# Kernel tuning notes

Measured on AMD Instinct MI355X. Metric: run time of the kernel, lower is better.

The kernel has to match this reference:

```python
import jax, jax.numpy as jnp
import numpy as np

N_NODES = 100000
N_EDGES = 1600000
N_GRAPHS = 256
F_IN = 38
HID = 64


def graph_conv(x, edge_index, w_rel, b_rel, w_root):
    # PyG GraphConv (aggr='add'): out = lin_rel(sum_{j in N(i)} x_j) + lin_root(x_i)
    src, dst = edge_index[0], edge_index[1]
    agg = jax.ops.segment_sum(x[src], dst, num_segments=N_NODES)  # [N, F]
    return agg @ w_rel + b_rel + x @ w_root


def setup_inputs() -> dict:
    key = jax.random.key(0)
    ks = jax.random.split(key, 10)
    x = jax.random.normal(ks[0], (N_NODES, F_IN), dtype=jnp.float32)
    edge_index = jax.random.randint(ks[1], (2, N_EDGES), 0, N_NODES, dtype=jnp.int64)
    batch = jnp.sort(jax.random.randint(ks[2], (N_NODES,), 0, N_GRAPHS, dtype=jnp.int64))
    s1 = 1.0 / np.sqrt(F_IN)
    s2 = 1.0 / np.sqrt(HID)
    w1_rel = jax.random.uniform(ks[3], (F_IN, HID), jnp.float32, -s1, s1)
    b1_rel = jax.random.uniform(ks[4], (HID,), jnp.float32, -s1, s1)
    w1_root = jax.random.uniform(ks[5], (F_IN, HID), jnp.float32, -s1, s1)
    w2_rel = jax.random.uniform(ks[6], (HID, HID), jnp.float32, -s2, s2)
    b2_rel = jax.random.uniform(ks[7], (HID,), jnp.float32, -s2, s2)
    w2_root = jax.random.uniform(ks[8], (HID, HID), jnp.float32, -s2, s2)
    return {"x": x, "edge_index": edge_index, "batch": batch,
            "w1_rel": w1_rel, "b1_rel": b1_rel, "w1_root": w1_root,
            "w2_rel": w2_rel, "b2_rel": b2_rel, "w2_root": w2_root}


def reference(x, edge_index, batch, w1_rel, b1_rel, w1_root, w2_rel, b2_rel, w2_root):
    h = graph_conv(x, edge_index, w1_rel, b1_rel, w1_root)
    h = jax.nn.relu(h)
    h = graph_conv(h, edge_index, w2_rel, b2_rel, w2_root)
    # global_mean_pool: segment mean over batch ids
    sums = jax.ops.segment_sum(h, batch, num_segments=N_GRAPHS)  # [G, HID]
    counts = jax.ops.segment_sum(jnp.ones((N_NODES,), h.dtype), batch, num_segments=N_GRAPHS)
    pooled = sums / jnp.maximum(counts, 1.0)[:, None]
    # dropout(p=0.5, training=False) is identity in eval mode
    return jax.nn.relu(pooled)
```

## Files before the change

### kernel.cpp

```cpp
#include <hip/hip_runtime.h>

#define N_NODES 100000
#define N_EDGES 1600000
#define N_GRAPHS 256
#define F_IN 38
#define F_PAD 40
#define HID 64
#define CAPD 48

#define NB   391
#define EPB  4096
#define NBLK 391
#define BCAP 4608

typedef unsigned short ushort;
typedef unsigned int uint;
typedef _Float16 h2 __attribute__((ext_vector_type(2)));

__device__ __forceinline__ h2 u2h(uint u) {
    union { uint u; h2 h; } v; v.u = u; return v.h;
}
__device__ __forceinline__ uint h2u(h2 h) {
    union { uint u; h2 h; } v; v.h = h; return v.u;
}
__device__ __forceinline__ ushort f2h_bits(float f) {
    union { _Float16 h; ushort s; } v; v.h = (_Float16)f; return v.s;
}
__device__ __forceinline__ int clampi(int v) {
    return (int)min((uint)v, (uint)N_NODES);
}

__global__ void pack_x_kernel(const float* __restrict__ x,
                              ushort* __restrict__ xb,
                              ushort* __restrict__ hb) {
    int tid = blockIdx.x * blockDim.x + threadIdx.x;
    if (tid < HID) hb[(N_NODES << 6) + tid] = 0;
    if (tid >= (N_NODES + 1) * F_PAD) return;
    int n = tid / F_PAD;
    int f = tid - n * F_PAD;
    float v = (n < N_NODES && f < F_IN) ? x[n * F_IN + f] : 0.0f;
    xb[tid] = f2h_bits(v);
}

__global__ void scatter_kernel(const int* __restrict__ src,
                               const int* __restrict__ dst,
                               int* __restrict__ gcur,
                               uint2* __restrict__ ebuf) {
    __shared__ int hist[NB];
    __shared__ int cur[NB];
    for (int i = threadIdx.x; i < NB; i += 256) hist[i] = 0;
    __syncthreads();
    const int base = blockIdx.x * EPB;
    int d[EPB / 256];
    #pragma unroll
    for (int i = 0; i < EPB / 256; ++i) {
        int e = base + i * 256 + threadIdx.x;
        d[i] = (e < N_EDGES) ? dst[e] : -1;
        if (d[i] >= 0) atomicAdd(&hist[d[i] >> 8], 1);
    }
    __syncthreads();
    for (int i = threadIdx.x; i < NB; i += 256) {
        int c = hist[i];
        cur[i] = (c > 0) ? atomicAdd(&gcur[i], c) : 0;
    }
    __syncthreads();
    #pragma unroll
    for (int i = 0; i < EPB / 256; ++i) {
        int e = base + i * 256 + threadIdx.x;
        if (d[i] >= 0) {
            int b = d[i] >> 8;
            int pos = atomicAdd(&cur[b], 1);
            if (pos < BCAP) ebuf[b * BCAP + pos] = make_uint2((uint)src[e], (uint)d[i]);
        }
    }
}

__global__ void build_kernel(const uint2* __restrict__ ebuf,
                             const int* __restrict__ gcur,
                             int* __restrict__ cnt,
                             int* __restrict__ slots) {
    __shared__ int cl[256];
    const int b = blockIdx.x;
    cl[threadIdx.x] = 0;
    __syncthreads();
    int e1 = gcur[b]; if (e1 > BCAP) e1 = BCAP;
    for (int idx = threadIdx.x; idx < e1; idx += 256) {
        uint2 e = ebuf[b * BCAP + idx];
        int pos = atomicAdd(&cl[e.y & 255], 1);
        if (pos < CAPD) slots[(int)e.y * CAPD + pos] = (int)e.x;
    }
    __syncthreads();
    int n = (b << 8) + threadIdx.x;
    if (n < N_NODES) cnt[n] = cl[threadIdx.x];
}

__global__ __launch_bounds__(256, 4) void layer1_kernel(
        const uint* __restrict__ xb32,
        const int* __restrict__ cnt,
        const int* __restrict__ slots,
        const float* __restrict__ w_rel,
        const float* __restrict__ b_rel,
        const float* __restrict__ w_root,
        const int* __restrict__ batch,
        ushort* __restrict__ hb,
        float* __restrict__ hsum) {
    __shared__ uint s_wrelp[20 * HID];
    __shared__ uint s_wrootp[20 * HID];
    __shared__ uint s_a[64][20];
    __shared__ uint s_x[64][20];
    for (int i = threadIdx.x; i < 20 * HID; i += 256) {
        int kk = i >> 6, cc = i & 63;
        int k0 = 2 * kk, k1 = 2 * kk + 1;
        float r0 = (k0 < F_IN) ? w_rel[k0 * HID + cc] : 0.f;
        float r1 = (k1 < F_IN) ? w_rel[k1 * HID + cc] : 0.f;
        float o0 = (k0 < F_IN) ? w_root[k0 * HID + cc] : 0.f;
        float o1 = (k1 < F_IN) ? w_root[k1 * HID + cc] : 0.f;
        s_wrelp[i]  = (uint)f2h_bits(r0) | ((uint)f2h_bits(r1) << 16);
        s_wrootp[i] = (uint)f2h_bits(o0) | ((uint)f2h_bits(o1) << 16);
    }
    const int wave = threadIdx.x >> 6, lane = threadIdx.x & 63;
    const int base = blockIdx.x * 64;

    for (int i = 0; i < 16; ++i) {
        int nl = wave * 16 + i;
        int n = base + nl;
        uint xv = 0;
        int dp = 0;
        if (n < N_NODES) {
            int deg = cnt[n]; if (deg > CAPD) deg = CAPD;
            dp = (deg + 15) & ~15; if (dp > CAPD) dp = CAPD;
            if (lane < 20) xv = xb32[n * 20 + lane];
        }
        h2 sum = {(_Float16)0, (_Float16)0};
        const int* sl = slots + n * CAPD;
        for (int j = 0; j < dp; j += 16) {
            int4 a4 = *(const int4*)(sl + j);
            int4 b4 = *(const int4*)(sl + j + 4);
            int4 c4 = *(const int4*)(sl + j + 8);
            int4 d4 = *(const int4*)(sl + j + 12);
            if (lane < 20) {
                uint v0 = xb32[clampi(a4.x) * 20 + lane];
                uint v1 = xb32[clampi(a4.y) * 20 + lane];
                uint v2 = xb32[clampi(a4.z) * 20 + lane];
                uint v3 = xb32[clampi(a4.w) * 20 + lane];
                uint v4 = xb32[clampi(b4.x) * 20 + lane];
                uint v5 = xb32[clampi(b4.y) * 20 + lane];
                uint v6 = xb32[clampi(b4.z) * 20 + lane];
                uint v7 = xb32[clampi(b4.w) * 20 + lane];
                uint v8 = xb32[clampi(c4.x) * 20 + lane];
                uint v9 = xb32[clampi(c4.y) * 20 + lane];
                uint va = xb32[clampi(c4.z) * 20 + lane];
                uint vb = xb32[clampi(c4.w) * 20 + lane];
                uint vc = xb32[clampi(d4.x) * 20 + lane];
                uint vd = xb32[clampi(d4.y) * 20 + lane];
                uint ve = xb32[clampi(d4.z) * 20 + lane];
                uint vf = xb32[clampi(d4.w) * 20 + lane];
                h2 t0 = (u2h(v0) + u2h(v1)) + (u2h(v2) + u2h(v3));
                h2 t1 = (u2h(v4) + u2h(v5)) + (u2h(v6) + u2h(v7));
                h2 t2 = (u2h(v8) + u2h(v9)) + (u2h(va) + u2h(vb));
                h2 t3 = (u2h(vc) + u2h(vd)) + (u2h(ve) + u2h(vf));
                sum += (t0 + t1) + (t2 + t3);
            }
        }
        if (lane < 20) {
            s_a[nl][lane] = h2u(sum);
            s_x[nl][lane] = xv;
        }
    }
    __syncthreads();

    const int c = lane, r = wave;
    const float bias = b_rel[c];
    float psum = 0.f;
    int cur_g = -1;
    for (int i = 0; i < 16; ++i) {
        int nl = r * 16 + i;
        int n = base + nl;
        if (n >= N_NODES) break;
        h2 acc = {(_Float16)0, (_Float16)0};
        #pragma unroll
        for (int k8 = 0; k8 < 5; ++k8) {
            uint4 pa = *(const uint4*)&s_a[nl][k8 * 4];
            uint4 px = *(const uint4*)&s_x[nl][k8 * 4];
            acc += u2h(pa.x) * u2h(s_wrelp[(k8 * 4 + 0) * HID + c]);
            acc += u2h(pa.y) * u2h(s_wrelp[(k8 * 4 + 1) * HID + c]);
            acc += u2h(pa.z) * u2h(s_wrelp[(k8 * 4 + 2) * HID + c]);
            acc += u2h(pa.w) * u2h(s_wrelp[(k8 * 4 + 3) * HID + c]);
            acc += u2h(px.x) * u2h(s_wrootp[(k8 * 4 + 0) * HID + c]);
            acc += u2h(px.y) * u2h(s_wrootp[(k8 * 4 + 1) * HID + c]);
            acc += u2h(px.z) * u2h(s_wrootp[(k8 * 4 + 2) * HID + c]);
            acc += u2h(px.w) * u2h(s_wrootp[(k8 * 4 + 3) * HID + c]);
        }
        float hv = fmaxf((float)acc.x + (float)acc.y + bias, 0.f);
        hb[(n << 6) + c] = f2h_bits(hv);
        int g = batch[n];
        if (g != cur_g) {
            if (cur_g >= 0) atomicAdd(&hsum[(cur_g << 6) + c], psum);
            psum = 0.f;
            cur_g = g;
        }
        psum += hv;
    }
    if (cur_g >= 0) atomicAdd(&hsum[(cur_g << 6) + c], psum);
}

__global__ __launch_bounds__(256, 4) void layer2_kernel(
        const uint* __restrict__ hb32,
        const int* __restrict__ cnt,
        const int* __restrict__ slots,
        const int* __restrict__ batch,
        float* __restrict__ esum) {
    const int wave = threadIdx.x >> 6, lane = threadIdx.x & 63;
    const int base = blockIdx.x * 64;

    float psum0 = 0.f, psum1 = 0.f;
    int cur_g = -1;
    for (int i = 0; i < 16; ++i) {
        int n = base + wave * 16 + i;
        if (n >= N_NODES) break;
        int deg = cnt[n]; if (deg > CAPD) deg = CAPD;
        int dp = (deg + 15) & ~15; if (dp > CAPD) dp = CAPD;
        h2 sum = {(_Float16)0, (_Float16)0};
        const int* sl = slots + n * CAPD;
        for (int j = 0; j < dp; j += 16) {
            int4 a4 = *(const int4*)(sl + j);
            int4 b4 = *(const int4*)(sl + j + 4);
            int4 c4 = *(const int4*)(sl + j + 8);
            int4 d4 = *(const int4*)(sl + j + 12);
            if (lane < 32) {
                uint v0 = hb32[(clampi(a4.x) << 5) + lane];
                uint v1 = hb32[(clampi(a4.y) << 5) + lane];
                uint v2 = hb32[(clampi(a4.z) << 5) + lane];
                uint v3 = hb32[(clampi(a4.w) << 5) + lane];
                uint v4 = hb32[(clampi(b4.x) << 5) + lane];
                uint v5 = hb32[(clampi(b4.y) << 5) + lane];
                uint v6 = hb32[(clampi(b4.z) << 5) + lane];
                uint v7 = hb32[(clampi(b4.w) << 5) + lane];
                uint v8 = hb32[(clampi(c4.x) << 5) + lane];
                uint v9 = hb32[(clampi(c4.y) << 5) + lane];
                uint va = hb32[(clampi(c4.z) << 5) + lane];
                uint vb = hb32[(clampi(c4.w) << 5) + lane];
                uint vc = hb32[(clampi(d4.x) << 5) + lane];
                uint vd = hb32[(clampi(d4.y) << 5) + lane];
                uint ve = hb32[(clampi(d4.z) << 5) + lane];
                uint vf = hb32[(clampi(d4.w) << 5) + lane];
                h2 t0 = (u2h(v0) + u2h(v1)) + (u2h(v2) + u2h(v3));
                h2 t1 = (u2h(v4) + u2h(v5)) + (u2h(v6) + u2h(v7));
                h2 t2 = (u2h(v8) + u2h(v9)) + (u2h(va) + u2h(vb));
                h2 t3 = (u2h(vc) + u2h(vd)) + (u2h(ve) + u2h(vf));
                sum += (t0 + t1) + (t2 + t3);
            }
        }
        if (lane < 32) {
            int g = batch[n];
            if (g != cur_g) {
                if (cur_g >= 0) {
                    atomicAdd(&esum[(cur_g << 6) + 2 * lane], psum0);
                    atomicAdd(&esum[(cur_g << 6) + 2 * lane + 1], psum1);
                }
                psum0 = 0.f; psum1 = 0.f;
                cur_g = g;
            }
            psum0 += (float)sum.x;
            psum1 += (float)sum.y;
        }
    }
    if (lane < 32 && cur_g >= 0) {
        atomicAdd(&esum[(cur_g << 6) + 2 * lane], psum0);
        atomicAdd(&esum[(cur_g << 6) + 2 * lane + 1], psum1);
    }
}

__global__ void finalize_kernel(const float* __restrict__ esum,
                                const float* __restrict__ hsum,
                                const float* __restrict__ w2_rel,
                                const float* __restrict__ w2_root,
                                const float* __restrict__ b2,
                                const int* __restrict__ batch,
                                float* __restrict__ out) {
    __shared__ float s_e[HID];
    __shared__ float s_h[HID];
    const int g = blockIdx.x;
    const int c = threadIdx.x;
    s_e[c] = esum[(g << 6) + c];
    s_h[c] = hsum[(g << 6) + c];
    __syncthreads();

    int lo = 0, hi = N_NODES;
    while (lo < hi) { int m = (lo + hi) >> 1; if (batch[m] < g) lo = m + 1; else hi = m; }
    int start = lo;
    hi = N_NODES;
    while (lo < hi) { int m = (lo + hi) >> 1; if (batch[m] < g + 1) lo = m + 1; else hi = m; }
    int cntg = lo - start;

    float acc = (float)cntg * b2[c];
    #pragma unroll
    for (int k = 0; k < HID; ++k) {
        acc += s_e[k] * w2_rel[k * HID + c];
        acc += s_h[k] * w2_root[k * HID + c];
    }
    float denom = cntg > 0 ? (float)cntg : 1.f;
    out[(g << 6) + c] = fmaxf(acc / denom, 0.f);
}

extern "C" void kernel_launch(void* const* d_in, const int* in_sizes, int n_in,
                              void* d_out, int out_size, void* d_ws, size_t ws_size,
                              hipStream_t stream) {
    const float* x       = (const float*)d_in[0];
    const int*   ei      = (const int*)  d_in[1];
    const int*   batch   = (const int*)  d_in[2];
    const float* w1_rel  = (const float*)d_in[3];
    const float* b1_rel  = (const float*)d_in[4];
    const float* w1_root = (const float*)d_in[5];
    const float* w2_rel  = (const float*)d_in[6];
    const float* b2_rel  = (const float*)d_in[7];
    const float* w2_root = (const float*)d_in[8];
    float* out = (float*)d_out;

    const int* src = ei;
    const int* dst = ei + N_EDGES;

    char* wsb = (char*)d_ws;
    int*    cnt   = (int*)   (wsb);
    float*  hsum  = (float*) (wsb + 400000);
    float*  esum  = (float*) (wsb + 465536);
    int*    gcur  = (int*)   (wsb + 531072);
    int*    slots = (int*)   (wsb + 532640);
    ushort* xb    = (ushort*)(wsb + 19732640);
    ushort* hb    = (ushort*)(wsb + 27732720);
    uint2*  ebuf  = (uint2*) (wsb + 19732640);

    hipMemsetAsync(wsb + 400000, 0, 132636, stream);

    scatter_kernel<<<NBLK, 256, 0, stream>>>(src, dst, gcur, ebuf);
    build_kernel<<<NB, 256, 0, stream>>>(ebuf, gcur, cnt, slots);

    {
        int total = (N_NODES + 1) * F_PAD;
        pack_x_kernel<<<(total + 255) / 256, 256, 0, stream>>>(x, xb, hb);
    }
    {
        int blocks = (N_NODES + 63) / 64;
        layer1_kernel<<<blocks, 256, 0, stream>>>((const uint*)xb, cnt, slots,
                                                  w1_rel, b1_rel, w1_root, batch,
                                                  hb, hsum);
    }
    {
        int blocks = (N_NODES + 63) / 64;
        layer2_kernel<<<blocks, 256, 0, stream>>>((const uint*)hb, cnt, slots,
                                                  batch, esum);
    }
    {
        finalize_kernel<<<N_GRAPHS, HID, 0, stream>>>(esum, hsum, w2_rel, w2_root,
                                                      b2_rel, batch, out);
    }
}
```

Measured before the change: 259.0 us.

## Use MFMA f16 for layer1 dense transform with concatenated rel/root weights

Replaces the per-lane packed-half dot products in layer1 with 16x16x32 f16 MFMA instructions. The rel and root weight matrices are concatenated along K into one padded shared tile (K=96), and each node row stores the aggregated features beside its own x features, read directly from the fp32 input. Accumulation moves to fp32, which changes numerics slightly. The epilogue is reorganised to match the MFMA output layout, giving four columns per lane. The gather phase likely dominates, so the gain may be limited.

After: 289.0 us. +11.6%, slower.

```diff
diff --git a/kernel.cpp b/kernel.cpp
--- a/kernel.cpp
+++ b/kernel.cpp
@@ -7,6 +7,7 @@
 #define F_PAD 40
 #define HID 64
 #define CAPD 48
+#define KROW 52
 
 #define NB   391
 #define EPB  4096
@@ -16,6 +17,8 @@
 typedef unsigned short ushort;
 typedef unsigned int uint;
 typedef _Float16 h2 __attribute__((ext_vector_type(2)));
+typedef _Float16 f16x8 __attribute__((ext_vector_type(8)));
+typedef float f32x4 __attribute__((ext_vector_type(4)));
 
 __device__ __forceinline__ h2 u2h(uint u) {
     union { uint u; h2 h; } v; v.u = u; return v.h;
@@ -95,6 +98,7 @@
 }
 
 __global__ __launch_bounds__(256, 4) void layer1_kernel(
+        const float* __restrict__ x,
         const uint* __restrict__ xb32,
         const int* __restrict__ cnt,
         const int* __restrict__ slots,
@@ -104,19 +108,23 @@
         const int* __restrict__ batch,
         ushort* __restrict__ hb,
         float* __restrict__ hsum) {
-    __shared__ uint s_wrelp[20 * HID];
-    __shared__ uint s_wrootp[20 * HID];
-    __shared__ uint s_a[64][20];
-    __shared__ uint s_x[64][20];
-    for (int i = threadIdx.x; i < 20 * HID; i += 256) {
-        int kk = i >> 6, cc = i & 63;
-        int k0 = 2 * kk, k1 = 2 * kk + 1;
-        float r0 = (k0 < F_IN) ? w_rel[k0 * HID + cc] : 0.f;
-        float r1 = (k1 < F_IN) ? w_rel[k1 * HID + cc] : 0.f;
-        float o0 = (k0 < F_IN) ? w_root[k0 * HID + cc] : 0.f;
-        float o1 = (k1 < F_IN) ? w_root[k1 * HID + cc] : 0.f;
-        s_wrelp[i]  = (uint)f2h_bits(r0) | ((uint)f2h_bits(r1) << 16);
-        s_wrootp[i] = (uint)f2h_bits(o0) | ((uint)f2h_bits(o1) << 16);
+    __shared__ __align__(16) uint s_w[64 * KROW];
+    __shared__ __align__(16) uint s_a[64 * KROW];
+
+    {
+        const int c = threadIdx.x >> 2;
+        const int k4 = threadIdx.x & 3;
+        #pragma unroll
+        for (int it = 0; it < 12; ++it) {
+            int kk = k4 + 4 * it;
+            int k0 = 2 * kk, k1 = 2 * kk + 1;
+            float v0 = 0.f, v1 = 0.f;
+            if (k0 < F_IN)                 v0 = w_rel[k0 * HID + c];
+            else if (k0 >= 48 && k0 < 86)  v0 = w_root[(k0 - 48) * HID + c];
+            if (k1 < F_IN)                 v1 = w_rel[k1 * HID + c];
+            else if (k1 >= 48 && k1 < 86)  v1 = w_root[(k1 - 48) * HID + c];
+            s_w[c * KROW + kk] = (uint)f2h_bits(v0) | ((uint)f2h_bits(v1) << 16);
+        }
     }
     const int wave = threadIdx.x >> 6, lane = threadIdx.x & 63;
     const int base = blockIdx.x * 64;
@@ -124,12 +132,10 @@
     for (int i = 0; i < 16; ++i) {
         int nl = wave * 16 + i;
         int n = base + nl;
-        uint xv = 0;
         int dp = 0;
         if (n < N_NODES) {
             int deg = cnt[n]; if (deg > CAPD) deg = CAPD;
             dp = (deg + 15) & ~15; if (dp > CAPD) dp = CAPD;
-            if (lane < 20) xv = xb32[n * 20 + lane];
         }
         h2 sum = {(_Float16)0, (_Float16)0};
         const int* sl = slots + n * CAPD;
@@ -162,46 +168,81 @@
                 sum += (t0 + t1) + (t2 + t3);
             }
         }
+        uint* row = s_a + nl * KROW;
         if (lane < 20) {
-            s_a[nl][lane] = h2u(sum);
-            s_x[nl][lane] = xv;
-        }
-    }
-    __syncthreads();
-
-    const int c = lane, r = wave;
-    const float bias = b_rel[c];
-    float psum = 0.f;
+            row[lane] = h2u(sum);
+        } else if (lane < 24) {
+            row[lane] = 0;
+        } else if (lane < 43) {
+            uint xv = 0;
+            int pidx = lane - 24;
+            if (n < N_NODES && pidx < 19) {
+                float2 xf = *(const float2*)(x + n * F_IN + 2 * pidx);
+                xv = (uint)f2h_bits(xf.x) | ((uint)f2h_bits(xf.y) << 16);
+            }
+            row[lane] = xv;
+        } else if (lane < 48) {
+            row[lane] = 0;
+        }
+    }
+    __syncthreads();
+
+    const int quad = lane >> 4, l16 = lane & 15;
+    const int mrow = wave * 16 + l16;
+    f32x4 acc0 = {0.f, 0.f, 0.f, 0.f};
+    f32x4 acc1 = acc0, acc2 = acc0, acc3 = acc0;
+    union U4H8 { uint4 u; f16x8 h; };
+    #pragma unroll
+    for (int q = 0; q < 3; ++q) {
+        const int ko = q * 16 + quad * 4;
+        U4H8 a;  a.u  = *(const uint4*)&s_a[mrow * KROW + ko];
+        U4H8 b0; b0.u = *(const uint4*)&s_w[(l16 + 0)  * KROW + ko];
+        U4H8 b1; b1.u = *(const uint4*)&s_w[(l16 + 16) * KROW + ko];
+        U4H8 b2; b2.u = *(const uint4*)&s_w[(l16 + 32) * KROW + ko];
+        U4H8 b3; b3.u = *(const uint4*)&s_w[(l16 + 48) * KROW + ko];
+        acc0 = __builtin_amdgcn_mfma_f32_16x16x32_f16(a.h, b0.h, acc0, 0, 0, 0);
+        acc1 = __builtin_amdgcn_mfma_f32_16x16x32_f16(a.h, b1.h, acc1, 0, 0, 0);
+        acc2 = __builtin_amdgcn_mfma_f32_16x16x32_f16(a.h, b2.h, acc2, 0, 0, 0);
+        acc3 = __builtin_amdgcn_mfma_f32_16x16x32_f16(a.h, b3.h, acc3, 0, 0, 0);
+    }
+
+    const int c0 = l16, c1 = l16 + 16, c2 = l16 + 32, c3 = l16 + 48;
+    const float bias0 = b_rel[c0], bias1 = b_rel[c1];
+    const float bias2 = b_rel[c2], bias3 = b_rel[c3];
+    float p0 = 0.f, p1 = 0.f, p2 = 0.f, p3 = 0.f;
     int cur_g = -1;
-    for (int i = 0; i < 16; ++i) {
-        int nl = r * 16 + i;
-        int n = base + nl;
-        if (n >= N_NODES) break;
-        h2 acc = {(_Float16)0, (_Float16)0};
-        #pragma unroll
-        for (int k8 = 0; k8 < 5; ++k8) {
-            uint4 pa = *(const uint4*)&s_a[nl][k8 * 4];
-            uint4 px = *(const uint4*)&s_x[nl][k8 * 4];
-            acc += u2h(pa.x) * u2h(s_wrelp[(k8 * 4 + 0) * HID + c]);
-            acc += u2h(pa.y) * u2h(s_wrelp[(k8 * 4 + 1) * HID + c]);
-            acc += u2h(pa.z) * u2h(s_wrelp[(k8 * 4 + 2) * HID + c]);
-            acc += u2h(pa.w) * u2h(s_wrelp[(k8 * 4 + 3) * HID + c]);
-            acc += u2h(px.x) * u2h(s_wrootp[(k8 * 4 + 0) * HID + c]);
-            acc += u2h(px.y) * u2h(s_wrootp[(k8 * 4 + 1) * HID + c]);
-            acc += u2h(px.z) * u2h(s_wrootp[(k8 * 4 + 2) * HID + c]);
-            acc += u2h(px.w) * u2h(s_wrootp[(k8 * 4 + 3) * HID + c]);
-        }
-        float hv = fmaxf((float)acc.x + (float)acc.y + bias, 0.f);
-        hb[(n << 6) + c] = f2h_bits(hv);
-        int g = batch[n];
-        if (g != cur_g) {
-            if (cur_g >= 0) atomicAdd(&hsum[(cur_g << 6) + c], psum);
-            psum = 0.f;
-            cur_g = g;
-        }
-        psum += hv;
-    }
-    if (cur_g >= 0) atomicAdd(&hsum[(cur_g << 6) + c], psum);
+    #pragma unroll
+    for (int r = 0; r < 4; ++r) {
+        int n = base + wave * 16 + quad * 4 + r;
+        if (n < N_NODES) {
+            float h0 = fmaxf(acc0[r] + bias0, 0.f);
+            float h1 = fmaxf(acc1[r] + bias1, 0.f);
+            float h2v = fmaxf(acc2[r] + bias2, 0.f);
+            float h3 = fmaxf(acc3[r] + bias3, 0.f);
+            hb[(n << 6) + c0] = f2h_bits(h0);
+            hb[(n << 6) + c1] = f2h_bits(h1);
+            hb[(n << 6) + c2] = f2h_bits(h2v);
+            hb[(n << 6) + c3] = f2h_bits(h3);
+            int g = batch[n];
+            if (g != cur_g) {
+                if (cur_g >= 0) {
+                    atomicAdd(&hsum[(cur_g << 6) + c0], p0);
+                    atomicAdd(&hsum[(cur_g << 6) + c1], p1);
+                    atomicAdd(&hsum[(cur_g << 6) + c2], p2);
+                    atomicAdd(&hsum[(cur_g << 6) + c3], p3);
+                }
+                p0 = p1 = p2 = p3 = 0.f;
+                cur_g = g;
+            }
+            p0 += h0; p1 += h1; p2 += h2v; p3 += h3;
+        }
+    }
+    if (cur_g >= 0) {
+        atomicAdd(&hsum[(cur_g << 6) + c0], p0);
+        atomicAdd(&hsum[(cur_g << 6) + c1], p1);
+        atomicAdd(&hsum[(cur_g << 6) + c2], p2);
+        atomicAdd(&hsum[(cur_g << 6) + c3], p3);
+    }
 }
 
 __global__ __launch_bounds__(256, 4) void layer2_kernel(
@@ -341,7 +382,7 @@
     }
     {
         int blocks = (N_NODES + 63) / 64;
-        layer1_kernel<<<blocks, 256, 0, stream>>>((const uint*)xb, cnt, slots,
+        layer1_kernel<<<blocks, 256, 0, stream>>>(x, (const uint*)xb, cnt, slots,
                                                   w1_rel, b1_rel, w1_root, batch,
                                                   hb, hsum);
     }
```
